# Performance work log

Measured on AMD Instinct MI355X. Metric: run time of the kernel, lower is better.

Reference implementation:

```python
import jax, jax.numpy as jnp
import numpy as np

N_NODES = 50000
N_EDGES = 800000
D_IN = 128
D_H = 128


def setup_inputs() -> dict:
    key = jax.random.key(0)
    ks = jax.random.split(key, 16)
    s = 0.05
    return {
        "x": jax.random.normal(ks[0], (N_NODES, D_IN), dtype=jnp.float32),
        "edge_index": jax.random.randint(ks[1], (2, N_EDGES), 0, N_NODES, dtype=jnp.int64),
        # GraphConv 1: out = aggr(x_j) @ W_rel + b + x @ W_root (lin_root has no bias in PyG)
        "W1_rel": jax.random.normal(ks[2], (D_IN, D_H), dtype=jnp.float32) * s,
        "b1": jnp.zeros((D_H,), dtype=jnp.float32),
        "W1_root": jax.random.normal(ks[3], (D_IN, D_H), dtype=jnp.float32) * s,
        # GraphConv 2
        "W2_rel": jax.random.normal(ks[4], (D_H, D_H), dtype=jnp.float32) * s,
        "b2": jnp.zeros((D_H,), dtype=jnp.float32),
        "W2_root": jax.random.normal(ks[5], (D_H, D_H), dtype=jnp.float32) * s,
        # mean head MLP: Linear(2H->H), ReLU, Linear(H->1)
        "Wm1": jax.random.normal(ks[6], (2 * D_H, D_H), dtype=jnp.float32) * s,
        "bm1": jnp.zeros((D_H,), dtype=jnp.float32),
        "Wm2": jax.random.normal(ks[7], (D_H, 1), dtype=jnp.float32) * s,
        "bm2": jnp.zeros((1,), dtype=jnp.float32),
        # logvar head MLP
        "Wv1": jax.random.normal(ks[8], (2 * D_H, D_H), dtype=jnp.float32) * s,
        "bv1": jnp.zeros((D_H,), dtype=jnp.float32),
        "Wv2": jax.random.normal(ks[9], (D_H, 1), dtype=jnp.float32) * s,
        "bv2": jnp.zeros((1,), dtype=jnp.float32),
    }


def _graph_conv(h, src, dst, n, W_rel, b, W_root):
    # PyG GraphConv (aggr='add'): out_i = (sum_{j->i} h_j) @ W_rel + b + h_i @ W_root
    agg = jax.ops.segment_sum(h[src], dst, num_segments=n)
    return agg @ W_rel + b + h @ W_root


def reference(x, edge_index, W1_rel, b1, W1_root, W2_rel, b2, W2_root,
              Wm1, bm1, Wm2, bm2, Wv1, bv1, Wv2, bv2):
    n = x.shape[0]
    src, dst = edge_index[0], edge_index[1]
    h = jax.nn.relu(_graph_conv(x, src, dst, n, W1_rel, b1, W1_root))
    h = jax.nn.relu(_graph_conv(h, src, dst, n, W2_rel, b2, W2_root))
    combined = jnp.concatenate([h[src], h[dst]], axis=1)  # [E, 2H]
    mean = jax.nn.relu(combined @ Wm1 + bm1) @ Wm2 + bm2  # [E, 1]
    logvar = jax.nn.relu(combined @ Wv1 + bv1) @ Wv2 + bv2
    var = jnp.exp(0.5 * logvar)
    return (mean, var)
```

## Files before the change

### kernel.cpp

```cpp
#include <hip/hip_runtime.h>
#include <cstdint>

#define NF 128

typedef unsigned int uint;
typedef short bf16x8 __attribute__((ext_vector_type(8)));
typedef float f32x4  __attribute__((ext_vector_type(4)));

__device__ __forceinline__ float2 ld2(const float* p) {
    return *reinterpret_cast<const float2*>(p);
}
__device__ __forceinline__ float bflo(uint u) { return __uint_as_float(u << 16); }
__device__ __forceinline__ float bfhi(uint u) { return __uint_as_float(u & 0xffff0000u); }
__device__ __forceinline__ uint f2bf_rne(float f) {
    uint u = __float_as_uint(f);
    return (u + 0x7fffu + ((u >> 16) & 1u)) >> 16;
}
__device__ __forceinline__ uint pack2bf(float a, float b) {
    return f2bf_rne(a) | (f2bf_rne(b) << 16);
}

__device__ __forceinline__ bf16x8 ldfrag(const uint* __restrict__ tab, int idx, int kb, int g) {
    const uint4 u = *reinterpret_cast<const uint4*>(&tab[(size_t)idx * 64 + kb * 16 + g * 4]);
    union { uint4 u4; bf16x8 b; } c; c.u4 = u; return c.b;
}

__global__ __launch_bounds__(256) void cast_bf16_k(const float* __restrict__ in,
                                                   uint* __restrict__ out, int npairs)
{
    int i = blockIdx.x * 256 + threadIdx.x;
    if (i >= npairs) return;
    float2 v = ld2(&in[(size_t)i * 2]);
    out[i] = pack2bf(v.x, v.y);
}

struct W8 {
    const float* src[8];
    uint*        dst[8];
};
__global__ __launch_bounds__(256) void wtpack_k(W8 p)
{
    int m = blockIdx.y;
    const float* s = p.src[m];
    uint* d = p.dst[m];
    int idx = blockIdx.x * 256 + threadIdx.x;
    int c   = idx >> 6;
    int kdw = idx & 63;
    float a = s[(size_t)(2 * kdw)     * NF + c];
    float b = s[(size_t)(2 * kdw + 1) * NF + c];
    d[(size_t)c * 64 + kdw] = pack2bf(a, b);
}

__global__ __launch_bounds__(256) void count_k(const int* __restrict__ ei,
                                               int* __restrict__ deg, int E)
{
    int e = blockIdx.x * 256 + threadIdx.x;
    if (e >= E) return;
    atomicAdd(&deg[ei[E + e]], 1);
}

__global__ __launch_bounds__(256) void scan1_k(const int* __restrict__ deg,
                                               int* __restrict__ rowptr,
                                               int* __restrict__ bsum, int N)
{
    int i = blockIdx.x * 256 + threadIdx.x;
    int v = (i < N) ? deg[i] : 0;
    int lane = threadIdx.x & 63;
    int wid  = threadIdx.x >> 6;
    int x = v;
#pragma unroll
    for (int off = 1; off < 64; off <<= 1) {
        int y = __shfl_up(x, off);
        if (lane >= off) x += y;
    }
    __shared__ int wsum[4];
    if (lane == 63) wsum[wid] = x;
    __syncthreads();
    int wadd = 0;
#pragma unroll
    for (int w = 0; w < 4; ++w) wadd += (w < wid) ? wsum[w] : 0;
    int incl = x + wadd;
    if (i < N) rowptr[i] = incl - v;
    if (threadIdx.x == 255) bsum[blockIdx.x] = incl;
}

__global__ __launch_bounds__(256) void scan2_k(int* __restrict__ bsum, int NB)
{
    int i = threadIdx.x;
    int v = (i < NB) ? bsum[i] : 0;
    int lane = threadIdx.x & 63;
    int wid  = threadIdx.x >> 6;
    int x = v;
#pragma unroll
    for (int off = 1; off < 64; off <<= 1) {
        int y = __shfl_up(x, off);
        if (lane >= off) x += y;
    }
    __shared__ int wsum[4];
    if (lane == 63) wsum[wid] = x;
    __syncthreads();
    int wadd = 0;
#pragma unroll
    for (int w = 0; w < 4; ++w) wadd += (w < wid) ? wsum[w] : 0;
    int incl = x + wadd;
    __syncthreads();
    if (i < NB) bsum[i] = incl - v;
}

__global__ __launch_bounds__(256) void scan3_k(const int* __restrict__ bsum,
                                               int* __restrict__ rowptr,
                                               int* __restrict__ cursor, int N, int E)
{
    int i = blockIdx.x * 256 + threadIdx.x;
    if (i == 0) rowptr[N] = E;
    if (i >= N) return;
    int r = rowptr[i] + bsum[blockIdx.x];
    rowptr[i] = r;
    cursor[i] = r;
}

__global__ __launch_bounds__(256) void fill_k(const int* __restrict__ ei,
                                              int* __restrict__ cursor,
                                              int* __restrict__ srclist,
                                              int* __restrict__ invpos, int E)
{
    int e = blockIdx.x * 256 + threadIdx.x;
    if (e >= E) return;
    int s = ei[e];
    int d = ei[E + e];
    int pos = atomicAdd(&cursor[d], 1);
    srclist[pos] = s;
    invpos[e] = pos;
}

__global__ __launch_bounds__(256) void agg2_k(const uint* __restrict__ Xb,
                                              const int* __restrict__ rowptr,
                                              const int* __restrict__ srclist,
                                              uint* __restrict__ AGGb, int N)
{
    int gid   = blockIdx.x * 256 + threadIdx.x;
    int wave  = gid >> 6;
    int lane  = gid & 63;
    int half  = lane >> 5;
    int hlane = lane & 31;
    int node  = wave * 2 + half;
    int nc    = min(node, N - 1);
    int beg = rowptr[nc];
    int end = rowptr[nc + 1];
    if (node >= N) { beg = 0; end = 0; }

    float ax = 0.f, ay = 0.f, az = 0.f, aw = 0.f;
    float bx = 0.f, by = 0.f, bz = 0.f, bw = 0.f;
    for (int j = beg; j < end; j += 2) {
        int  ok1 = (j + 1 < end);
        int  s0 = srclist[j];
        int  s1 = ok1 ? srclist[j + 1] : s0;
        uint2 w0 = *reinterpret_cast<const uint2*>(&Xb[(size_t)s0 * 64 + hlane * 2]);
        uint2 w1 = *reinterpret_cast<const uint2*>(&Xb[(size_t)s1 * 64 + hlane * 2]);
        ax += bflo(w0.x); ay += bfhi(w0.x); az += bflo(w0.y); aw += bfhi(w0.y);
        if (ok1) { bx += bflo(w1.x); by += bfhi(w1.x); bz += bflo(w1.y); bw += bfhi(w1.y); }
    }
    if (node < N) {
        uint2 o;
        o.x = pack2bf(ax + bx, ay + by);
        o.y = pack2bf(az + bz, aw + bw);
        *reinterpret_cast<uint2*>(&AGGb[(size_t)node * 64 + hlane * 2]) = o;
    }
}

__global__ __launch_bounds__(256) void dualgemm_mfma_k(
    const uint* __restrict__ Aa, const uint* __restrict__ WaT,
    const uint* __restrict__ Ab, const uint* __restrict__ WbT,
    const float* __restrict__ bias, uint* __restrict__ C, int Nrows)
{
    const int lane = threadIdx.x & 63;
    const int wid  = threadIdx.x >> 6;
    const int g    = lane >> 4;
    const int r15  = lane & 15;
    const int rowBase = blockIdx.x * 64 + wid * 16;
    if (rowBase >= Nrows) return;
    const int arow = rowBase + r15;

    bf16x8 ba[4], bb[4];
#pragma unroll
    for (int kb = 0; kb < 4; ++kb) {
        ba[kb] = ldfrag(Aa, arow, kb, g);
        bb[kb] = ldfrag(Ab, arow, kb, g);
    }

#pragma unroll
    for (int ct = 0; ct < 8; ++ct) {
        const int wcol = ct * 16 + r15;
        f32x4 acc = {0.f, 0.f, 0.f, 0.f};
#pragma unroll
        for (int kb = 0; kb < 4; ++kb)
            acc = __builtin_amdgcn_mfma_f32_16x16x32_bf16(ldfrag(WaT, wcol, kb, g), ba[kb], acc, 0, 0, 0);
#pragma unroll
        for (int kb = 0; kb < 4; ++kb)
            acc = __builtin_amdgcn_mfma_f32_16x16x32_bf16(ldfrag(WbT, wcol, kb, g), bb[kb], acc, 0, 0, 0);

        const int colBase = ct * 16 + g * 4;
        float4 bs = *reinterpret_cast<const float4*>(&bias[colBase]);
        float v0 = fmaxf(acc[0] + bs.x, 0.f);
        float v1 = fmaxf(acc[1] + bs.y, 0.f);
        float v2 = fmaxf(acc[2] + bs.z, 0.f);
        float v3 = fmaxf(acc[3] + bs.w, 0.f);
        uint2 pk;
        pk.x = pack2bf(v0, v1);
        pk.y = pack2bf(v2, v3);
        *reinterpret_cast<uint2*>(&C[(size_t)arow * 64 + ct * 8 + g * 2]) = pk;
    }
}

__global__ __launch_bounds__(256) void headgemm_mfma_k(
    const uint* __restrict__ Hb,
    const uint* __restrict__ WPt, const uint* __restrict__ WQt,
    const uint* __restrict__ WRt, const uint* __restrict__ WSt,
    const float* __restrict__ bm1, const float* __restrict__ bv1,
    uint* __restrict__ PRb, uint* __restrict__ QSb, int Nrows)
{
    const int lane = threadIdx.x & 63;
    const int wid  = threadIdx.x >> 6;
    const int g    = lane >> 4;
    const int r15  = lane & 15;
    const int rowBase = blockIdx.x * 64 + wid * 16;
    if (rowBase >= Nrows) return;
    const int arow = rowBase + r15;

    bf16x8 hb[4];
#pragma unroll
    for (int kb = 0; kb < 4; ++kb) hb[kb] = ldfrag(Hb, arow, kb, g);

#pragma unroll
    for (int ct = 0; ct < 8; ++ct) {
        const int wcol = ct * 16 + r15;
        f32x4 aP = {0.f,0.f,0.f,0.f}, aQ = {0.f,0.f,0.f,0.f};
        f32x4 aR = {0.f,0.f,0.f,0.f}, aS = {0.f,0.f,0.f,0.f};
#pragma unroll
        for (int kb = 0; kb < 4; ++kb) {
            aP = __builtin_amdgcn_mfma_f32_16x16x32_bf16(ldfrag(WPt, wcol, kb, g), hb[kb], aP, 0, 0, 0);
            aQ = __builtin_amdgcn_mfma_f32_16x16x32_bf16(ldfrag(WQt, wcol, kb, g), hb[kb], aQ, 0, 0, 0);
            aR = __builtin_amdgcn_mfma_f32_16x16x32_bf16(ldfrag(WRt, wcol, kb, g), hb[kb], aR, 0, 0, 0);
            aS = __builtin_amdgcn_mfma_f32_16x16x32_bf16(ldfrag(WSt, wcol, kb, g), hb[kb], aS, 0, 0, 0);
        }
        const int colBase = ct * 16 + g * 4;
        float4 bmv = *reinterpret_cast<const float4*>(&bm1[colBase]);
        float4 bvv = *reinterpret_cast<const float4*>(&bv1[colBase]);
        float p0 = aP[0] + bmv.x, p1 = aP[1] + bmv.y, p2 = aP[2] + bmv.z, p3 = aP[3] + bmv.w;
        float r0 = aR[0] + bvv.x, r1 = aR[1] + bvv.y, r2 = aR[2] + bvv.z, r3 = aR[3] + bvv.w;
        uint4 pr, qs;
        pr.x = pack2bf(p0, p1);     pr.y = pack2bf(r0, r1);
        pr.z = pack2bf(p2, p3);     pr.w = pack2bf(r2, r3);
        qs.x = pack2bf(aQ[0], aQ[1]); qs.y = pack2bf(aS[0], aS[1]);
        qs.z = pack2bf(aQ[2], aQ[3]); qs.w = pack2bf(aS[2], aS[3]);
        *reinterpret_cast<uint4*>(&PRb[(size_t)arow * 128 + ct * 16 + g * 4]) = pr;
        *reinterpret_cast<uint4*>(&QSb[(size_t)arow * 128 + ct * 16 + g * 4]) = qs;
    }
}

__global__ __launch_bounds__(256) void edge_head3_k(
    const uint* __restrict__ PRb, const uint* __restrict__ QSb,
    const int* __restrict__ rowptr, const int* __restrict__ srclist,
    const float* __restrict__ Wm2, const float* __restrict__ Wv2,
    float2* __restrict__ tmp, int N)
{
    int gid   = blockIdx.x * 256 + threadIdx.x;
    int node  = gid >> 6;
    int lane  = gid & 63;
    int half  = lane >> 5;
    int hlane = lane & 31;
    if (node >= N) return;
    int beg = rowptr[node];
    int end = rowptr[node + 1];
    if (beg == end) return;

    uint4 qs4 = *reinterpret_cast<const uint4*>(&QSb[(size_t)node * 128 + hlane * 4]);
    float q0 = bflo(qs4.x), q1 = bfhi(qs4.x);
    float s0 = bflo(qs4.y), s1 = bfhi(qs4.y);
    float q2 = bflo(qs4.z), q3 = bfhi(qs4.z);
    float s2 = bflo(qs4.w), s3 = bfhi(qs4.w);

    float4 wm = *reinterpret_cast<const float4*>(&Wm2[hlane * 4]);
    float4 wv = *reinterpret_cast<const float4*>(&Wv2[hlane * 4]);

    for (int base = beg; base < end; base += 2) {
        int p  = base + half;
        int pc = min(p, end - 1);
        int src = srclist[pc];
        uint4 pr4 = *reinterpret_cast<const uint4*>(&PRb[(size_t)src * 128 + hlane * 4]);
        float P0 = bflo(pr4.x), P1 = bfhi(pr4.x);
        float R0 = bflo(pr4.y), R1 = bfhi(pr4.y);
        float P2 = bflo(pr4.z), P3 = bfhi(pr4.z);
        float R2 = bflo(pr4.w), R3 = bfhi(pr4.w);

        float pm = fmaf(fmaxf(P0 + q0, 0.f), wm.x,
                   fmaf(fmaxf(P1 + q1, 0.f), wm.y,
                   fmaf(fmaxf(P2 + q2, 0.f), wm.z,
                        fmaxf(P3 + q3, 0.f) * wm.w)));
        float pv = fmaf(fmaxf(R0 + s0, 0.f), wv.x,
                   fmaf(fmaxf(R1 + s1, 0.f), wv.y,
                   fmaf(fmaxf(R2 + s2, 0.f), wv.z,
                        fmaxf(R3 + s3, 0.f) * wv.w)));

        pm += __shfl_xor(pm, 16);
        pv += __shfl_xor(pv, 16);
        float c = (hlane & 16) ? pv : pm;
        c += __shfl_xor(c, 8);
        c += __shfl_xor(c, 4);
        c += __shfl_xor(c, 2);
        c += __shfl_xor(c, 1);
        float other = __shfl(c, (lane & 32) + 16);
        if (hlane == 0 && p < end) tmp[p] = make_float2(c, other);
    }
}

__global__ __launch_bounds__(256) void permute_k(
    const float2* __restrict__ tmp, const int* __restrict__ invpos,
    const float* __restrict__ bm2, const float* __restrict__ bv2,
    float* __restrict__ mean_out, float* __restrict__ var_out, int E)
{
    int e = blockIdx.x * 256 + threadIdx.x;
    if (e >= E) return;
    float2 t = tmp[invpos[e]];
    mean_out[e] = t.x + bm2[0];
    var_out[e]  = expf(0.5f * (t.y + bv2[0]));
}

extern "C" void kernel_launch(void* const* d_in, const int* in_sizes, int n_in,
                              void* d_out, int out_size, void* d_ws, size_t ws_size,
                              hipStream_t stream)
{
    const float* x       = (const float*)d_in[0];
    const int*   ei      = (const int*)d_in[1];
    const float* W1_rel  = (const float*)d_in[2];
    const float* b1      = (const float*)d_in[3];
    const float* W1_root = (const float*)d_in[4];
    const float* W2_rel  = (const float*)d_in[5];
    const float* b2      = (const float*)d_in[6];
    const float* W2_root = (const float*)d_in[7];
    const float* Wm1     = (const float*)d_in[8];
    const float* bm1     = (const float*)d_in[9];
    const float* Wm2     = (const float*)d_in[10];
    const float* bm2     = (const float*)d_in[11];
    const float* Wv1     = (const float*)d_in[12];
    const float* bv1     = (const float*)d_in[13];
    const float* Wv2     = (const float*)d_in[14];
    const float* bv2     = (const float*)d_in[15];

    const int N = in_sizes[0] / NF;
    const int E = in_sizes[1] / 2;

    const size_t SZ16 = (size_t)N * NF * 2;

    char* base = (char*)d_ws;
    uint* x_b  = (uint*)(base);
    uint* h2b  = (uint*)(base);
    uint* h1b  = (uint*)(base + SZ16);
    uint* AGGb = (uint*)(base + 2 * SZ16);
    uint* PRb  = (uint*)(base + SZ16);
    uint* QSb  = (uint*)(base + 3 * SZ16);

    char* wts = base + 5 * SZ16;
    uint* wt[8];
    for (int i = 0; i < 8; ++i) wt[i] = (uint*)(wts + (size_t)i * 32768);

    char* csr = wts + 8 * 32768;
    int* deg     = (int*)(csr);
    int* rowptr  = (int*)(csr + (size_t)(N + 64) * 4);
    int* cursor  = (int*)(csr + (size_t)(N + 64) * 8);
    int* srclist = (int*)(csr + (size_t)(N + 64) * 12);
    int* invpos  = srclist + E;
    float2* tmp  = (float2*)(invpos + E);
    int* bsum    = (int*)(tmp + E);

    float* out_mean = (float*)d_out;
    float* out_var  = out_mean + E;

    dim3 blk(256);
    dim3 eGrid((E + 255) / 256);
    dim3 mfmaGrid((N + 63) / 64);
    dim3 nodeGrid((unsigned)(((size_t)N * 64 + 255) / 256));
    dim3 node2Grid((unsigned)((((size_t)(N + 1) / 2) * 64 + 255) / 256));
    const int NB = (N + 255) / 256;
    dim3 scanGrid(NB);

    hipLaunchKernelGGL(cast_bf16_k, nodeGrid, blk, 0, stream, x, x_b, N * 64);

    W8 wp;
    wp.src[0] = W1_rel;            wp.dst[0] = wt[0];
    wp.src[1] = W1_root;           wp.dst[1] = wt[1];
    wp.src[2] = W2_rel;            wp.dst[2] = wt[2];
    wp.src[3] = W2_root;           wp.dst[3] = wt[3];
    wp.src[4] = Wm1;               wp.dst[4] = wt[4];
    wp.src[5] = Wm1 + NF * NF;     wp.dst[5] = wt[5];
    wp.src[6] = Wv1;               wp.dst[6] = wt[6];
    wp.src[7] = Wv1 + NF * NF;     wp.dst[7] = wt[7];
    hipLaunchKernelGGL(wtpack_k, dim3(32, 8), blk, 0, stream, wp);

    hipMemsetAsync(deg, 0, (size_t)N * 4, stream);
    hipLaunchKernelGGL(count_k, eGrid, blk, 0, stream, ei, deg, E);
    hipLaunchKernelGGL(scan1_k, scanGrid, blk, 0, stream, deg, rowptr, bsum, N);
    hipLaunchKernelGGL(scan2_k, dim3(1), blk, 0, stream, bsum, NB);
    hipLaunchKernelGGL(scan3_k, scanGrid, blk, 0, stream, bsum, rowptr, cursor, N, E);
    hipLaunchKernelGGL(fill_k, eGrid, blk, 0, stream, ei, cursor, srclist, invpos, E);

    hipLaunchKernelGGL(agg2_k, node2Grid, blk, 0, stream, x_b, rowptr, srclist, AGGb, N);
    hipLaunchKernelGGL(dualgemm_mfma_k, mfmaGrid, blk, 0, stream,
                       AGGb, wt[0], x_b, wt[1], b1, h1b, N);

    hipLaunchKernelGGL(agg2_k, node2Grid, blk, 0, stream, h1b, rowptr, srclist, AGGb, N);
    hipLaunchKernelGGL(dualgemm_mfma_k, mfmaGrid, blk, 0, stream,
                       AGGb, wt[2], h1b, wt[3], b2, h2b, N);

    hipLaunchKernelGGL(headgemm_mfma_k, mfmaGrid, blk, 0, stream,
                       h2b, wt[4], wt[5], wt[6], wt[7], bm1, bv1, PRb, QSb, N);

    hipLaunchKernelGGL(edge_head3_k, nodeGrid, blk, 0, stream,
                       PRb, QSb, rowptr, srclist, Wm2, Wv2, tmp, N);

    hipLaunchKernelGGL(permute_k, eGrid, blk, 0, stream,
                       tmp, invpos, bm2, bv2, out_mean, out_var, E);
}
```

Before: 504.0 us.

## Software-prefetch gathers in aggregation and edge head; double row tiles in MFMA GEMMs

The neighbour-aggregation and edge-head loops now load the next iteration's source indices and feature rows before doing the current accumulation. This double-buffering is meant to hide gather latency. The dual-GEMM and head-GEMM kernels now have each wave compute two 16-row tiles, so each weight fragment load feeds two MFMAs and weight-load traffic per row is halved. In exchange, register pressure rises, which may lower occupancy, and the GEMM grid has half as many blocks.

```diff
diff --git a/kernel.cpp b/kernel.cpp
--- a/kernel.cpp
+++ b/kernel.cpp
@@ -151,14 +151,30 @@
 
     float ax = 0.f, ay = 0.f, az = 0.f, aw = 0.f;
     float bx = 0.f, by = 0.f, bz = 0.f, bw = 0.f;
+
+    uint2 w0 = make_uint2(0, 0), w1 = make_uint2(0, 0);
+    int ok1 = 0;
+    if (beg < end) {
+        int s0 = srclist[beg];
+        ok1 = (beg + 1 < end);
+        int s1 = ok1 ? srclist[beg + 1] : s0;
+        w0 = *reinterpret_cast<const uint2*>(&Xb[(size_t)s0 * 64 + hlane * 2]);
+        w1 = *reinterpret_cast<const uint2*>(&Xb[(size_t)s1 * 64 + hlane * 2]);
+    }
     for (int j = beg; j < end; j += 2) {
-        int  ok1 = (j + 1 < end);
-        int  s0 = srclist[j];
-        int  s1 = ok1 ? srclist[j + 1] : s0;
-        uint2 w0 = *reinterpret_cast<const uint2*>(&Xb[(size_t)s0 * 64 + hlane * 2]);
-        uint2 w1 = *reinterpret_cast<const uint2*>(&Xb[(size_t)s1 * 64 + hlane * 2]);
+        int jn = j + 2;
+        uint2 nw0 = w0, nw1 = w1;
+        int nok1 = 0;
+        if (jn < end) {
+            int s0 = srclist[jn];
+            nok1 = (jn + 1 < end);
+            int s1 = nok1 ? srclist[jn + 1] : s0;
+            nw0 = *reinterpret_cast<const uint2*>(&Xb[(size_t)s0 * 64 + hlane * 2]);
+            nw1 = *reinterpret_cast<const uint2*>(&Xb[(size_t)s1 * 64 + hlane * 2]);
+        }
         ax += bflo(w0.x); ay += bfhi(w0.x); az += bflo(w0.y); aw += bfhi(w0.y);
         if (ok1) { bx += bflo(w1.x); by += bfhi(w1.x); bz += bflo(w1.y); bw += bfhi(w1.y); }
+        w0 = nw0; w1 = nw1; ok1 = nok1;
     }
     if (node < N) {
         uint2 o;
@@ -177,38 +193,49 @@
     const int wid  = threadIdx.x >> 6;
     const int g    = lane >> 4;
     const int r15  = lane & 15;
-    const int rowBase = blockIdx.x * 64 + wid * 16;
+    const int rowBase = blockIdx.x * 128 + wid * 32;
     if (rowBase >= Nrows) return;
-    const int arow = rowBase + r15;
-
-    bf16x8 ba[4], bb[4];
+    const int arow0 = rowBase + r15;
+    const int t1ok  = (rowBase + 16) < Nrows;
+    const int arow1 = t1ok ? (rowBase + 16 + r15) : arow0;
+
+    bf16x8 ba0[4], bb0[4], ba1[4], bb1[4];
 #pragma unroll
     for (int kb = 0; kb < 4; ++kb) {
-        ba[kb] = ldfrag(Aa, arow, kb, g);
-        bb[kb] = ldfrag(Ab, arow, kb, g);
+        ba0[kb] = ldfrag(Aa, arow0, kb, g);
+        bb0[kb] = ldfrag(Ab, arow0, kb, g);
+        ba1[kb] = ldfrag(Aa, arow1, kb, g);
+        bb1[kb] = ldfrag(Ab, arow1, kb, g);
     }
 
 #pragma unroll
     for (int ct = 0; ct < 8; ++ct) {
         const int wcol = ct * 16 + r15;
-        f32x4 acc = {0.f, 0.f, 0.f, 0.f};
-#pragma unroll
-        for (int kb = 0; kb < 4; ++kb)
-            acc = __builtin_amdgcn_mfma_f32_16x16x32_bf16(ldfrag(WaT, wcol, kb, g), ba[kb], acc, 0, 0, 0);
-#pragma unroll
-        for (int kb = 0; kb < 4; ++kb)
-            acc = __builtin_amdgcn_mfma_f32_16x16x32_bf16(ldfrag(WbT, wcol, kb, g), bb[kb], acc, 0, 0, 0);
+        f32x4 a0 = {0.f, 0.f, 0.f, 0.f};
+        f32x4 a1 = {0.f, 0.f, 0.f, 0.f};
+#pragma unroll
+        for (int kb = 0; kb < 4; ++kb) {
+            bf16x8 wf = ldfrag(WaT, wcol, kb, g);
+            a0 = __builtin_amdgcn_mfma_f32_16x16x32_bf16(wf, ba0[kb], a0, 0, 0, 0);
+            a1 = __builtin_amdgcn_mfma_f32_16x16x32_bf16(wf, ba1[kb], a1, 0, 0, 0);
+        }
+#pragma unroll
+        for (int kb = 0; kb < 4; ++kb) {
+            bf16x8 wf = ldfrag(WbT, wcol, kb, g);
+            a0 = __builtin_amdgcn_mfma_f32_16x16x32_bf16(wf, bb0[kb], a0, 0, 0, 0);
+            a1 = __builtin_amdgcn_mfma_f32_16x16x32_bf16(wf, bb1[kb], a1, 0, 0, 0);
+        }
 
         const int colBase = ct * 16 + g * 4;
         float4 bs = *reinterpret_cast<const float4*>(&bias[colBase]);
-        float v0 = fmaxf(acc[0] + bs.x, 0.f);
-        float v1 = fmaxf(acc[1] + bs.y, 0.f);
-        float v2 = fmaxf(acc[2] + bs.z, 0.f);
-        float v3 = fmaxf(acc[3] + bs.w, 0.f);
-        uint2 pk;
-        pk.x = pack2bf(v0, v1);
-        pk.y = pack2bf(v2, v3);
-        *reinterpret_cast<uint2*>(&C[(size_t)arow * 64 + ct * 8 + g * 2]) = pk;
+        uint2 pk0, pk1;
+        pk0.x = pack2bf(fmaxf(a0[0] + bs.x, 0.f), fmaxf(a0[1] + bs.y, 0.f));
+        pk0.y = pack2bf(fmaxf(a0[2] + bs.z, 0.f), fmaxf(a0[3] + bs.w, 0.f));
+        pk1.x = pack2bf(fmaxf(a1[0] + bs.x, 0.f), fmaxf(a1[1] + bs.y, 0.f));
+        pk1.y = pack2bf(fmaxf(a1[2] + bs.z, 0.f), fmaxf(a1[3] + bs.w, 0.f));
+        *reinterpret_cast<uint2*>(&C[(size_t)arow0 * 64 + ct * 8 + g * 2]) = pk0;
+        if (t1ok)
+            *reinterpret_cast<uint2*>(&C[(size_t)arow1 * 64 + ct * 8 + g * 2]) = pk1;
     }
 }
 
@@ -223,38 +250,63 @@
     const int wid  = threadIdx.x >> 6;
     const int g    = lane >> 4;
     const int r15  = lane & 15;
-    const int rowBase = blockIdx.x * 64 + wid * 16;
+    const int rowBase = blockIdx.x * 128 + wid * 32;
     if (rowBase >= Nrows) return;
-    const int arow = rowBase + r15;
-
-    bf16x8 hb[4];
-#pragma unroll
-    for (int kb = 0; kb < 4; ++kb) hb[kb] = ldfrag(Hb, arow, kb, g);
+    const int arow0 = rowBase + r15;
+    const int t1ok  = (rowBase + 16) < Nrows;
+    const int arow1 = t1ok ? (rowBase + 16 + r15) : arow0;
+
+    bf16x8 hb0[4], hb1[4];
+#pragma unroll
+    for (int kb = 0; kb < 4; ++kb) {
+        hb0[kb] = ldfrag(Hb, arow0, kb, g);
+        hb1[kb] = ldfrag(Hb, arow1, kb, g);
+    }
 
 #pragma unroll
     for (int ct = 0; ct < 8; ++ct) {
         const int wcol = ct * 16 + r15;
-        f32x4 aP = {0.f,0.f,0.f,0.f}, aQ = {0.f,0.f,0.f,0.f};
-        f32x4 aR = {0.f,0.f,0.f,0.f}, aS = {0.f,0.f,0.f,0.f};
+        f32x4 aP0 = {0.f,0.f,0.f,0.f}, aQ0 = {0.f,0.f,0.f,0.f};
+        f32x4 aR0 = {0.f,0.f,0.f,0.f}, aS0 = {0.f,0.f,0.f,0.f};
+        f32x4 aP1 = {0.f,0.f,0.f,0.f}, aQ1 = {0.f,0.f,0.f,0.f};
+        f32x4 aR1 = {0.f,0.f,0.f,0.f}, aS1 = {0.f,0.f,0.f,0.f};
 #pragma unroll
         for (int kb = 0; kb < 4; ++kb) {
-            aP = __builtin_amdgcn_mfma_f32_16x16x32_bf16(ldfrag(WPt, wcol, kb, g), hb[kb], aP, 0, 0, 0);
-            aQ = __builtin_amdgcn_mfma_f32_16x16x32_bf16(ldfrag(WQt, wcol, kb, g), hb[kb], aQ, 0, 0, 0);
-            aR = __builtin_amdgcn_mfma_f32_16x16x32_bf16(ldfrag(WRt, wcol, kb, g), hb[kb], aR, 0, 0, 0);
-            aS = __builtin_amdgcn_mfma_f32_16x16x32_bf16(ldfrag(WSt, wcol, kb, g), hb[kb], aS, 0, 0, 0);
+            bf16x8 wP = ldfrag(WPt, wcol, kb, g);
+            bf16x8 wQ = ldfrag(WQt, wcol, kb, g);
+            bf16x8 wR = ldfrag(WRt, wcol, kb, g);
+            bf16x8 wS = ldfrag(WSt, wcol, kb, g);
+            aP0 = __builtin_amdgcn_mfma_f32_16x16x32_bf16(wP, hb0[kb], aP0, 0, 0, 0);
+            aP1 = __builtin_amdgcn_mfma_f32_16x16x32_bf16(wP, hb1[kb], aP1, 0, 0, 0);
+            aQ0 = __builtin_amdgcn_mfma_f32_16x16x32_bf16(wQ, hb0[kb], aQ0, 0, 0, 0);
+            aQ1 = __builtin_amdgcn_mfma_f32_16x16x32_bf16(wQ, hb1[kb], aQ1, 0, 0, 0);
+            aR0 = __builtin_amdgcn_mfma_f32_16x16x32_bf16(wR, hb0[kb], aR0, 0, 0, 0);
+            aR1 = __builtin_amdgcn_mfma_f32_16x16x32_bf16(wR, hb1[kb], aR1, 0, 0, 0);
+            aS0 = __builtin_amdgcn_mfma_f32_16x16x32_bf16(wS, hb0[kb], aS0, 0, 0, 0);
+            aS1 = __builtin_amdgcn_mfma_f32_16x16x32_bf16(wS, hb1[kb], aS1, 0, 0, 0);
         }
         const int colBase = ct * 16 + g * 4;
         float4 bmv = *reinterpret_cast<const float4*>(&bm1[colBase]);
         float4 bvv = *reinterpret_cast<const float4*>(&bv1[colBase]);
-        float p0 = aP[0] + bmv.x, p1 = aP[1] + bmv.y, p2 = aP[2] + bmv.z, p3 = aP[3] + bmv.w;
-        float r0 = aR[0] + bvv.x, r1 = aR[1] + bvv.y, r2 = aR[2] + bvv.z, r3 = aR[3] + bvv.w;
-        uint4 pr, qs;
-        pr.x = pack2bf(p0, p1);     pr.y = pack2bf(r0, r1);
-        pr.z = pack2bf(p2, p3);     pr.w = pack2bf(r2, r3);
-        qs.x = pack2bf(aQ[0], aQ[1]); qs.y = pack2bf(aS[0], aS[1]);
-        qs.z = pack2bf(aQ[2], aQ[3]); qs.w = pack2bf(aS[2], aS[3]);
-        *reinterpret_cast<uint4*>(&PRb[(size_t)arow * 128 + ct * 16 + g * 4]) = pr;
-        *reinterpret_cast<uint4*>(&QSb[(size_t)arow * 128 + ct * 16 + g * 4]) = qs;
+        uint4 pr0, qs0, pr1, qs1;
+        pr0.x = pack2bf(aP0[0] + bmv.x, aP0[1] + bmv.y);
+        pr0.y = pack2bf(aR0[0] + bvv.x, aR0[1] + bvv.y);
+        pr0.z = pack2bf(aP0[2] + bmv.z, aP0[3] + bmv.w);
+        pr0.w = pack2bf(aR0[2] + bvv.z, aR0[3] + bvv.w);
+        qs0.x = pack2bf(aQ0[0], aQ0[1]); qs0.y = pack2bf(aS0[0], aS0[1]);
+        qs0.z = pack2bf(aQ0[2], aQ0[3]); qs0.w = pack2bf(aS0[2], aS0[3]);
+        pr1.x = pack2bf(aP1[0] + bmv.x, aP1[1] + bmv.y);
+        pr1.y = pack2bf(aR1[0] + bvv.x, aR1[1] + bvv.y);
+        pr1.z = pack2bf(aP1[2] + bmv.z, aP1[3] + bmv.w);
+        pr1.w = pack2bf(aR1[2] + bvv.z, aR1[3] + bvv.w);
+        qs1.x = pack2bf(aQ1[0], aQ1[1]); qs1.y = pack2bf(aS1[0], aS1[1]);
+        qs1.z = pack2bf(aQ1[2], aQ1[3]); qs1.w = pack2bf(aS1[2], aS1[3]);
+        *reinterpret_cast<uint4*>(&PRb[(size_t)arow0 * 128 + ct * 16 + g * 4]) = pr0;
+        *reinterpret_cast<uint4*>(&QSb[(size_t)arow0 * 128 + ct * 16 + g * 4]) = qs0;
+        if (t1ok) {
+            *reinterpret_cast<uint4*>(&PRb[(size_t)arow1 * 128 + ct * 16 + g * 4]) = pr1;
+            *reinterpret_cast<uint4*>(&QSb[(size_t)arow1 * 128 + ct * 16 + g * 4]) = qs1;
+        }
     }
 }
 
@@ -283,15 +335,23 @@
     float4 wm = *reinterpret_cast<const float4*>(&Wm2[hlane * 4]);
     float4 wv = *reinterpret_cast<const float4*>(&Wv2[hlane * 4]);
 
+    int p0 = beg + half;
+    int src0 = srclist[min(p0, end - 1)];
+    uint4 pr_cur = *reinterpret_cast<const uint4*>(&PRb[(size_t)src0 * 128 + hlane * 4]);
+
     for (int base = beg; base < end; base += 2) {
-        int p  = base + half;
-        int pc = min(p, end - 1);
-        int src = srclist[pc];
-        uint4 pr4 = *reinterpret_cast<const uint4*>(&PRb[(size_t)src * 128 + hlane * 4]);
-        float P0 = bflo(pr4.x), P1 = bfhi(pr4.x);
-        float R0 = bflo(pr4.y), R1 = bfhi(pr4.y);
-        float P2 = bflo(pr4.z), P3 = bfhi(pr4.z);
-        float R2 = bflo(pr4.w), R3 = bfhi(pr4.w);
+        int p = base + half;
+        uint4 pr_next = pr_cur;
+        if (base + 2 < end) {
+            int pn = base + 2 + half;
+            int srcn = srclist[min(pn, end - 1)];
+            pr_next = *reinterpret_cast<const uint4*>(&PRb[(size_t)srcn * 128 + hlane * 4]);
+        }
+
+        float P0 = bflo(pr_cur.x), P1 = bfhi(pr_cur.x);
+        float R0 = bflo(pr_cur.y), R1 = bfhi(pr_cur.y);
+        float P2 = bflo(pr_cur.z), P3 = bfhi(pr_cur.z);
+        float R2 = bflo(pr_cur.w), R3 = bfhi(pr_cur.w);
 
         float pm = fmaf(fmaxf(P0 + q0, 0.f), wm.x,
                    fmaf(fmaxf(P1 + q1, 0.f), wm.y,
@@ -311,6 +371,8 @@
         c += __shfl_xor(c, 1);
         float other = __shfl(c, (lane & 32) + 16);
         if (hlane == 0 && p < end) tmp[p] = make_float2(c, other);
+
+        pr_cur = pr_next;
     }
 }
 
@@ -378,7 +440,7 @@
 
     dim3 blk(256);
     dim3 eGrid((E + 255) / 256);
-    dim3 mfmaGrid((N + 63) / 64);
+    dim3 mfmaGrid((N + 127) / 128);
     dim3 nodeGrid((unsigned)(((size_t)N * 64 + 255) / 256));
     dim3 node2Grid((unsigned)((((size_t)(N + 1) / 2) * 64 + 255) / 256));
     const int NB = (N + 255) / 256;
```

New measurement: 450.4 us. 1.12x faster.
